# Kernel tuning notes

Measured on AMD Instinct MI355X. Metric: run time of the kernel, lower is better.

The kernel has to match this reference:

```python
import jax, jax.numpy as jnp
import numpy as np

N, E, DIN, HID, H, ED = 50000, 800000, 128, 64, 4, 5
Z_IDX = 3          # impedance column
PHYS_W = 1.0       # physics_weight
NEG_SLOPE = 0.2    # GATv2 leaky_relu slope


def gat_layer(x, src, dst, ea, Wl, bl, Wr, br, We, att, temp, bias, concat):
    """PhysicsGATv2Conv (add_self_loops=False, eval mode / no dropout)."""
    n = x.shape[0]
    Hh, C = att.shape
    xl = (x @ Wl + bl).reshape(n, Hh, C)   # lin_l -> source features
    xr = (x @ Wr + br).reshape(n, Hh, C)   # lin_r -> target features
    # physics-enhanced edge attr: overwrite last column with temp * w / |Z|
    z = jnp.clip(ea[:, Z_IDX], 1e-6, None)
    ea = ea.at[:, -1].set(temp * PHYS_W / z)
    e = (ea @ We).reshape(-1, Hh, C)       # lin_edge (no bias)
    m = jax.nn.leaky_relu(xl[src] + xr[dst] + e, NEG_SLOPE)  # [E,H,C]
    logit = jnp.einsum('ehc,hc->eh', m, att)                 # [E,H]
    # segment softmax over incoming edges of each target node
    lmax = jax.ops.segment_max(logit, dst, num_segments=n)
    w = jnp.exp(logit - lmax[dst])
    den = jax.ops.segment_sum(w, dst, num_segments=n)
    a = w / (den[dst] + 1e-16)
    out = jax.ops.segment_sum(xl[src] * a[:, :, None], dst, num_segments=n)
    out = out.reshape(n, Hh * C) if concat else out.mean(axis=1)
    return out + bias


def layer_norm(x, w, b):
    mu = x.mean(-1, keepdims=True)
    v = ((x - mu) ** 2).mean(-1, keepdims=True)
    return (x - mu) * jax.lax.rsqrt(v + 1e-5) * w + b


def setup_inputs() -> dict:
    key = jax.random.key(0)
    ks = iter(jax.random.split(key, 40))
    nk = lambda: next(ks)
    d = {}
    d['x'] = jax.random.normal(nk(), (N, DIN), jnp.float32)
    d['edge_index'] = jax.random.randint(nk(), (2, E), 0, N)
    d['edge_attr'] = jax.random.uniform(nk(), (E, ED), jnp.float32)
    hd = HID * H
    cfg = [(DIN, True), (hd, True), (hd, False)]
    for i, (din, concat) in enumerate(cfg):
        dout = hd if concat else HID
        d[f'Wl{i}'] = jax.random.normal(nk(), (din, hd), jnp.float32) / np.sqrt(din)
        d[f'bl{i}'] = 0.01 * jax.random.normal(nk(), (hd,), jnp.float32)
        d[f'Wr{i}'] = jax.random.normal(nk(), (din, hd), jnp.float32) / np.sqrt(din)
        d[f'br{i}'] = 0.01 * jax.random.normal(nk(), (hd,), jnp.float32)
        d[f'We{i}'] = jax.random.normal(nk(), (ED, hd), jnp.float32) / np.sqrt(ED)
        d[f'att{i}'] = jax.random.normal(nk(), (H, HID), jnp.float32) / np.sqrt(HID)
        d[f'temp{i}'] = jnp.float32(1.0)
        d[f'bias{i}'] = 0.01 * jax.random.normal(nk(), (dout,), jnp.float32)
        d[f'lnw{i}'] = jnp.ones((dout,), jnp.float32)
        d[f'lnb{i}'] = jnp.zeros((dout,), jnp.float32)
    d['pw0'] = jax.random.normal(nk(), (DIN, hd), jnp.float32) / np.sqrt(DIN)
    d['pb0'] = jnp.zeros((hd,), jnp.float32)
    d['pw2'] = jax.random.normal(nk(), (hd, HID), jnp.float32) / np.sqrt(hd)
    d['pb2'] = jnp.zeros((HID,), jnp.float32)
    return d


def reference(x, edge_index, edge_attr,
              Wl0, bl0, Wr0, br0, We0, att0, temp0, bias0, lnw0, lnb0,
              Wl1, bl1, Wr1, br1, We1, att1, temp1, bias1, lnw1, lnb1,
              Wl2, bl2, Wr2, br2, We2, att2, temp2, bias2, lnw2, lnb2,
              pw0, pb0, pw2, pb2):
    src, dst = edge_index[0], edge_index[1]
    # layer 0: 128 -> 256 (concat), residual projected
    h = gat_layer(x, src, dst, edge_attr, Wl0, bl0, Wr0, br0, We0, att0, temp0, bias0, True)
    h = layer_norm(h, lnw0, lnb0) + (x @ pw0 + pb0)
    h = jax.nn.elu(h)
    # layer 1: 256 -> 256 (concat), identity residual
    h1 = gat_layer(h, src, dst, edge_attr, Wl1, bl1, Wr1, br1, We1, att1, temp1, bias1, True)
    h = layer_norm(h1, lnw1, lnb1) + h
    h = jax.nn.elu(h)
    # layer 2: 256 -> 64 (head-mean), residual projected, no activation
    h2 = gat_layer(h, src, dst, edge_attr, Wl2, bl2, Wr2, br2, We2, att2, temp2, bias2, False)
    out = layer_norm(h2, lnw2, lnb2) + (h @ pw2 + pb2)
    return out
```

## Files before the change

kernel.cpp:

```cpp
#include <hip/hip_runtime.h>
#include <math.h>

#define NN 50000
#define EE 800000
#define NB 196

typedef _Float16 half8 __attribute__((ext_vector_type(8)));
typedef _Float16 hv4  __attribute__((ext_vector_type(4)));
typedef _Float16 hv2  __attribute__((ext_vector_type(2)));
typedef __fp16 fp16v2 __attribute__((ext_vector_type(2)));
typedef float floatx16 __attribute__((ext_vector_type(16)));
typedef float fv4 __attribute__((ext_vector_type(4)));

__device__ __forceinline__ float fexp2(float x) { return __builtin_amdgcn_exp2f(x); }

template<int CTRL>
__device__ __forceinline__ float dppadd(float x) {
    int t = __builtin_amdgcn_update_dpp(0, __float_as_int(x), CTRL, 0xf, 0xf, false);
    return x + __int_as_float(t);
}
__device__ __forceinline__ float red16(float x) {
    x = dppadd<0x121>(x);
    x = dppadd<0x122>(x);
    x = dppadd<0x124>(x);
    x = dppadd<0x128>(x);
    return x;
}

__device__ __forceinline__ unsigned int dup16(float x) {
    unsigned short b = __builtin_bit_cast(unsigned short, (_Float16)x);
    return (unsigned int)b * 0x10001u;
}
__device__ __forceinline__ unsigned int duph(float x) {
#if __has_builtin(__builtin_amdgcn_cvt_pkrtz)
    fp16v2 p = __builtin_amdgcn_cvt_pkrtz(x, x);
    return __builtin_bit_cast(unsigned int, p);
#else
    return dup16(x);
#endif
}
__device__ __forceinline__ hv4 b4(unsigned int u) {
    hv2 p = __builtin_bit_cast(hv2, u);
    return (hv4){p[0], p[1], p[0], p[1]};
}
__device__ __forceinline__ float dot4h(hv4 a, hv4 b, float c) {
    hv2 al = {a[0], a[1]}, ah = {a[2], a[3]};
    hv2 bl = {b[0], b[1]}, bh = {b[2], b[3]};
#if __has_builtin(__builtin_amdgcn_fdot2)
    return __builtin_amdgcn_fdot2(al, bl, __builtin_amdgcn_fdot2(ah, bh, c, false), false);
#else
    return c + (float)a[0]*(float)b[0] + (float)a[1]*(float)b[1]
             + (float)a[2]*(float)b[2] + (float)a[3]*(float)b[3];
#endif
}

__global__ __launch_bounds__(256) void swizzleA(
    const float* __restrict__ A, _Float16* __restrict__ Asw, int M, int K)
{
    int wave = threadIdx.x >> 6, lane = threadIdx.x & 63;
    int tile = blockIdx.x;
    int kc = blockIdx.y * 4 + wave;
    int KC = K >> 4;
    if (kc >= KC) return;
    int row = tile * 32 + (lane & 31);
    int k0 = kc * 16 + (lane >> 5) * 8;
    float4 v0 = make_float4(0.f, 0.f, 0.f, 0.f);
    float4 v1 = make_float4(0.f, 0.f, 0.f, 0.f);
    if (row < M) {
        const float* p = A + (size_t)row * K + k0;
        v0 = *(const float4*)p;
        v1 = *(const float4*)(p + 4);
    }
    half8 o;
    o[0] = (_Float16)v0.x; o[1] = (_Float16)v0.y;
    o[2] = (_Float16)v0.z; o[3] = (_Float16)v0.w;
    o[4] = (_Float16)v1.x; o[5] = (_Float16)v1.y;
    o[6] = (_Float16)v1.z; o[7] = (_Float16)v1.w;
    *(half8*)(Asw + (((size_t)tile * KC + kc) * 64 + lane) * 8) = o;
}

__global__ __launch_bounds__(256) void prep_weights(
    const float* __restrict__ s0, const float* __restrict__ s1,
    const float* __restrict__ s2, const float* __restrict__ s3,
    const float* __restrict__ s4, const float* __restrict__ s5,
    const float* __restrict__ s6, const float* __restrict__ s7,
    _Float16* __restrict__ catB0, _Float16* __restrict__ catB1,
    _Float16* __restrict__ catB2,
    const float* __restrict__ bl0, const float* __restrict__ br0,
    const float* __restrict__ pb0, const float* __restrict__ bl1,
    const float* __restrict__ br1, const float* __restrict__ bl2,
    const float* __restrict__ br2, const float* __restrict__ pb2,
    float* __restrict__ cb0, float* __restrict__ cb1, float* __restrict__ cb2,
    const float* __restrict__ We0a, const float* __restrict__ We1a,
    const float* __restrict__ We2a, const float* __restrict__ att0a,
    const float* __restrict__ att1a, const float* __restrict__ att2a,
    _Float16* __restrict__ Weh)
{
    int b = blockIdx.x;
    if (b == 192) {
        const float* Ws[3] = {We0a, We1a, We2a};
        const float* As[3] = {att0a, att1a, att2a};
        for (int t = threadIdx.x; t < 4608; t += 256) {
            int l = t / 1536, o = t - l * 1536;
            float v = (o < 1280) ? Ws[l][o] : As[l][o - 1280];
            Weh[t] = (_Float16)v;
        }
        return;
    }
    if (b >= 184) {
        int t = (b - 184) * 256 + threadIdx.x;
        if (t < 768) {
            cb0[t] = (t < 256) ? bl0[t] : (t < 512) ? br0[t - 256] : pb0[t - 512];
        } else if (t < 1280) {
            int u = t - 768;
            cb1[u] = (u < 256) ? bl1[u] : br1[u - 256];
        } else if (t < 1856) {
            int u = t - 1280;
            cb2[u] = (u < 256) ? bl2[u] : (u < 512) ? br2[u - 256] : pb2[u - 512];
        }
        return;
    }
    int wave = threadIdx.x >> 6, lane = threadIdx.x & 63;
    int pair = b * 4 + wave;
    const int cum[9] = {0, 64, 128, 192, 320, 448, 576, 704, 736};
    int job = 0;
    while (pair >= cum[job + 1]) ++job;
    const float* srcs[8] = {s0, s1, s2, s3, s4, s5, s6, s7};
    const int KCs[8] = {8, 8, 8, 16, 16, 16, 16, 16};
    const int NCs[8] = {256, 256, 256, 256, 256, 256, 256, 64};
    const int ntb[8] = {0, 8, 16, 0, 8, 0, 8, 16};
    _Float16* dsts[8] = {catB0, catB0, catB0, catB1, catB1, catB2, catB2, catB2};
    int p = pair - cum[job];
    int KC = KCs[job], NC = NCs[job];
    int nt = p / KC, kc = p - nt * KC;
    int n = (nt >> 1) * 64 + ((lane & 31) * 2) + (nt & 1);
    int k0 = kc * 16 + (lane >> 5) * 8;
    const float* B = srcs[job];
    half8 o;
#pragma unroll
    for (int jj = 0; jj < 8; ++jj)
        o[jj] = (_Float16)B[(size_t)(k0 + jj) * NC + n];
    int ntG = ntb[job] + nt;
    *(half8*)(dsts[job] + (((size_t)ntG * KC + kc) * 64 + lane) * 8) = o;
}

__global__ __launch_bounds__(256) void gemm_mfma(
    const _Float16* __restrict__ Asw, const _Float16* __restrict__ Bsw,
    const float* __restrict__ bias, _Float16* __restrict__ C,
    int M, int K, int NC)
{
    const int wave = threadIdx.x >> 6, lane = threadIdx.x & 63;
    const int KC = K >> 4;
    const int rt0 = blockIdx.x * 2;
    const int NG = NC >> 6;
    int g = blockIdx.y * 4 + wave;
    if (g >= NG) g = NG - 1;

    const half8* Ap0 = (const half8*)Asw + (size_t)rt0 * KC * 64 + lane;
    const half8* Ap1 = Ap0 + (size_t)KC * 64;
    const half8* Bp0 = (const half8*)Bsw + (size_t)(2 * g) * KC * 64 + lane;
    const half8* Bp1 = Bp0 + (size_t)KC * 64;

    floatx16 accE0 = {0.f}, accE1 = {0.f}, accO0 = {0.f}, accO1 = {0.f};

#pragma unroll 4
    for (int kc = 0; kc < KC; ++kc) {
        half8 a0 = Ap0[(size_t)kc * 64];
        half8 a1 = Ap1[(size_t)kc * 64];
        half8 b0 = Bp0[(size_t)kc * 64];
        half8 b1 = Bp1[(size_t)kc * 64];
        accE0 = __builtin_amdgcn_mfma_f32_32x32x16_f16(a0, b0, accE0, 0, 0, 0);
        accE1 = __builtin_amdgcn_mfma_f32_32x32x16_f16(a1, b0, accE1, 0, 0, 0);
        accO0 = __builtin_amdgcn_mfma_f32_32x32x16_f16(a0, b1, accO0, 0, 0, 0);
        accO1 = __builtin_amdgcn_mfma_f32_32x32x16_f16(a1, b1, accO1, 0, 0, 0);
    }

    const int nlane = lane & 31, hs = lane >> 5;
    int colb = g * 64 + nlane * 2;
    float be = bias[colb], bo = bias[colb + 1];
#pragma unroll
    for (int r = 0; r < 16; ++r) {
        int rowin = (r & 3) + 8 * (r >> 2) + 4 * hs;
        int row0 = rt0 * 32 + rowin;
        int row1 = row0 + 32;
        if (row0 < M) {
            hv2 pe;
            pe[0] = (_Float16)(accE0[r] + be);
            pe[1] = (_Float16)(accO0[r] + bo);
            *(hv2*)(C + (size_t)row0 * NC + colb) = pe;
        }
        if (row1 < M) {
            hv2 po;
            po[0] = (_Float16)(accE1[r] + be);
            po[1] = (_Float16)(accO1[r] + bo);
            *(hv2*)(C + (size_t)row1 * NC + colb) = po;
        }
    }
}

__global__ __launch_bounds__(256) void hist_kernel(const int* __restrict__ dst,
                                                   int* __restrict__ deg)
{
    int e = blockIdx.x * 256 + threadIdx.x;
    if (e < EE) atomicAdd(&deg[dst[e]], 1);
}

__global__ __launch_bounds__(256) void scan_local(const int* __restrict__ deg,
                                                  int* __restrict__ rowoff,
                                                  int* __restrict__ part)
{
    __shared__ int sd[256];
    int tid = threadIdx.x;
    int i = blockIdx.x * 256 + tid;
    int v = (i < NN) ? deg[i] : 0;
    sd[tid] = v;
    __syncthreads();
    for (int off = 1; off < 256; off <<= 1) {
        int t = (tid >= off) ? sd[tid - off] : 0;
        __syncthreads();
        sd[tid] += t;
        __syncthreads();
    }
    if (i < NN) rowoff[i] = sd[tid] - v;
    if (tid == 255) part[blockIdx.x] = sd[255];
}

__global__ __launch_bounds__(256) void scan_part(int* __restrict__ part,
                                                 int* __restrict__ rowoff)
{
    __shared__ int sd[256];
    int tid = threadIdx.x;
    int v = (tid < NB) ? part[tid] : 0;
    sd[tid] = v;
    __syncthreads();
    for (int off = 1; off < 256; off <<= 1) {
        int t = (tid >= off) ? sd[tid - off] : 0;
        __syncthreads();
        sd[tid] += t;
        __syncthreads();
    }
    if (tid < NB) part[tid] = sd[tid] - v;
    if (tid == 0) rowoff[NN] = EE;
}

__global__ __launch_bounds__(256) void scan_add(int* __restrict__ rowoff,
                                                const int* __restrict__ part,
                                                int* __restrict__ cursor)
{
    int i = blockIdx.x * 256 + threadIdx.x;
    if (i < NN) {
        rowoff[i] += part[blockIdx.x];
        cursor[i] = 0;
    }
}

__global__ __launch_bounds__(256) void scatter_kernel(
    const int* __restrict__ src, const int* __restrict__ dst,
    const float* __restrict__ ea, const int* __restrict__ rowoff,
    int* __restrict__ cursor, int2* __restrict__ sep,
    unsigned int* __restrict__ apk)
{
    int e = blockIdx.x * 256 + threadIdx.x;
    if (e < EE) {
        int d = dst[e];
        int pos = rowoff[d] + atomicAdd(&cursor[d], 1);
        const float* p = ea + (size_t)e * 5;
        int2 o2;
        o2.x = src[e];
        o2.y = __float_as_int(1.0f / fmaxf(p[3], 1e-6f));
        sep[pos] = o2;
        uint4 o;
        o.x = dup16(p[0]); o.y = dup16(p[1]);
        o.z = dup16(p[2]); o.w = dup16(p[3]);
        *(uint4*)(apk + (size_t)pos * 4) = o;
    }
}

__global__ __launch_bounds__(256) void build_qtab(
    const int2* __restrict__ sep,
    const float* __restrict__ tA, unsigned int* __restrict__ qA,
    const float* __restrict__ tB, unsigned int* __restrict__ qB)
{
    int e = blockIdx.x * 256 + threadIdx.x;
    if (e >= EE) return;
    float er = __int_as_float(sep[e].y);
    {
        float q = tA[0] * er;
        float qs = fminf(q, 64.f);
        float inv = (q > 64.f) ? 64.f * __builtin_amdgcn_rcpf(q) : 1.0f;
        float sl = fmaxf(q * 0.015625f, 1.f) * 1.44269504088896340736f;
        uint4 o;
        o.x = dup16(qs);
        o.y = dup16(inv);
        o.z = __builtin_bit_cast(unsigned int, sl);
        o.w = 0u;
        *(uint4*)(qA + (size_t)e * 4) = o;
    }
    if (qB) {
        float q = tB[0] * er;
        float qs = fminf(q, 64.f);
        float inv = (q > 64.f) ? 64.f * __builtin_amdgcn_rcpf(q) : 1.0f;
        float sl = fmaxf(q * 0.015625f, 1.f) * 1.44269504088896340736f;
        uint4 o;
        o.x = dup16(qs);
        o.y = dup16(inv);
        o.z = __builtin_bit_cast(unsigned int, sl);
        o.w = 0u;
        *(uint4*)(qB + (size_t)e * 4) = o;
    }
}

template<int MODE, int RSTRIDE>
__global__ __launch_bounds__(256) void fused_attn_ln(
    const int* __restrict__ rowoff, const int2* __restrict__ sep,
    const unsigned int* __restrict__ apk, const unsigned int* __restrict__ qtab,
    const _Float16* __restrict__ xlp, const _Float16* __restrict__ Wh,
    const float* __restrict__ bias, const float* __restrict__ lnw,
    const float* __restrict__ lnb,
    const _Float16* __restrict__ residH, _Float16* __restrict__ h16,
    float* __restrict__ outF, _Float16* __restrict__ aswOut)
{
    int v = __builtin_amdgcn_readfirstlane(blockIdx.x * 4 + (threadIdx.x >> 6));
    int lane = threadIdx.x & 63;
    if (v >= NN) return;
    int grp = lane >> 4;
    int sub = lane & 15;
    int j = grp * 64 + sub * 4;

    hv4 ww0h = *(const hv4*)(Wh + j);
    hv4 ww1h = *(const hv4*)(Wh + 256 + j);
    hv4 ww2h = *(const hv4*)(Wh + 512 + j);
    hv4 ww3h = *(const hv4*)(Wh + 768 + j);
    hv4 ww4h = *(const hv4*)(Wh + 1024 + j);
    hv4 atvh = *(const hv4*)(Wh + 1280 + j);
    hv4 xrvh = *(const hv4*)(xlp + (size_t)v * RSTRIDE + 256 + j);
    const _Float16 s02 = (_Float16)0.2f;
    const hv4 sl02 = {s02, s02, s02, s02};
    const float L2E = 1.44269504088896340736f;

    float mxd = -INFINITY, dend = 0.f;
    fv4 acc = {0.f, 0.f, 0.f, 0.f};

    int beg = __builtin_amdgcn_readfirstlane(rowoff[v]);
    int end = __builtin_amdgcn_readfirstlane(rowoff[v + 1]);
    int i = beg;
    for (; i + 4 <= end; i += 4) {
        int s[4]; uint4 ap[4], qt[4]; hv4 xh[4]; float l[4];
#pragma unroll
        for (int u = 0; u < 4; ++u) {
            int2 sv = sep[i + u];
            s[u] = __builtin_amdgcn_readfirstlane(sv.x);
            ap[u] = *(const uint4*)(apk + (size_t)(i + u) * 4);
            qt[u] = *(const uint4*)(qtab + (size_t)(i + u) * 4);
        }
#pragma unroll
        for (int u = 0; u < 4; ++u)
            xh[u] = *(const hv4*)(xlp + (size_t)s[u] * RSTRIDE + j);
#pragma unroll
        for (int u = 0; u < 4; ++u) {
            hv4 t = xh[u] + xrvh;
            t += b4(ap[u].x) * ww0h;
            t += b4(ap[u].y) * ww1h;
            t += b4(ap[u].z) * ww2h;
            t += b4(ap[u].w) * ww3h;
            hv4 m = b4(qt[u].x) * ww4h;
            m += b4(qt[u].y) * t;
            hv4 mn = m * sl02;
            m = __builtin_elementwise_max(m, mn);
            l[u] = dot4h(m, atvh, 0.f);
        }
#pragma unroll
        for (int u = 0; u < 4; ++u)
            l[u] = red16(l[u]) * __builtin_bit_cast(float, qt[u].z);
        float nm = fmaxf(fmaxf(l[0], l[1]), fmaxf(l[2], l[3]));
        nm = fmaxf(nm, mxd);
        float sc = fexp2(mxd - nm);
        float e0 = fexp2(l[0] - nm);
        float e1 = fexp2(l[1] - nm);
        float e2 = fexp2(l[2] - nm);
        float e3 = fexp2(l[3] - nm);
        mxd = nm;
        dend = dend * sc + ((e0 + e1) + (e2 + e3));
        hv4 X = xh[0] * b4(duph(e0));
        X += xh[1] * b4(duph(e1));
        X += xh[2] * b4(duph(e2));
        X += xh[3] * b4(duph(e3));
        fv4 Xf = __builtin_convertvector(X, fv4);
        acc = acc * sc + Xf;
    }
    for (; i < end; ++i) {
        int2 sv = sep[i];
        int s0 = __builtin_amdgcn_readfirstlane(sv.x);
        uint4 ap = *(const uint4*)(apk + (size_t)i * 4);
        uint4 qt = *(const uint4*)(qtab + (size_t)i * 4);
        hv4 xh = *(const hv4*)(xlp + (size_t)s0 * RSTRIDE + j);
        hv4 t = xh + xrvh;
        t += b4(ap.x) * ww0h;
        t += b4(ap.y) * ww1h;
        t += b4(ap.z) * ww2h;
        t += b4(ap.w) * ww3h;
        hv4 m = b4(qt.x) * ww4h;
        m += b4(qt.y) * t;
        hv4 mn = m * sl02;
        m = __builtin_elementwise_max(m, mn);
        float l0 = dot4h(m, atvh, 0.f);
        l0 = red16(l0) * __builtin_bit_cast(float, qt.z);
        float nm = fmaxf(mxd, l0);
        float sc = fexp2(mxd - nm);
        float e0 = fexp2(l0 - nm);
        mxd = nm;
        dend = dend * sc + e0;
        fv4 xf = __builtin_convertvector(xh, fv4);
        acc = acc * sc + xf * e0;
    }

    float inv = __builtin_amdgcn_rcpf(dend + 1e-16f);
    if (MODE <= 1) {
        fv4 bb = *(const fv4*)(bias + j);
        fv4 o = acc * inv + bb;
        float s  = (o[0] + o[1]) + (o[2] + o[3]);
        fv4 oq = o * o;
        float s2 = (oq[0] + oq[1]) + (oq[2] + oq[3]);
        s = red16(s);   s += __shfl_xor(s, 16, 64);  s += __shfl_xor(s, 32, 64);
        s2 = red16(s2); s2 += __shfl_xor(s2, 16, 64); s2 += __shfl_xor(s2, 32, 64);
        float mu = s * (1.f / 256.f);
        float var = s2 * (1.f / 256.f) - mu * mu;
        float rs = __builtin_amdgcn_rsqf(var + 1e-5f);
        fv4 lw = *(const fv4*)(lnw + j);
        fv4 lb = *(const fv4*)(lnb + j);
        fv4 rr;
        if (MODE == 0)
            rr = __builtin_convertvector(
                *(const hv4*)(residH + (size_t)v * RSTRIDE + j), fv4);
        else
            rr = __builtin_convertvector(
                *(const hv4*)(residH + (size_t)v * 256 + j), fv4);
        fv4 y = (o - mu) * rs * lw + lb + rr;
        y[0] = (y[0] > 0.f) ? y[0] : fexp2(y[0] * L2E) - 1.f;
        y[1] = (y[1] > 0.f) ? y[1] : fexp2(y[1] * L2E) - 1.f;
        y[2] = (y[2] > 0.f) ? y[2] : fexp2(y[2] * L2E) - 1.f;
        y[3] = (y[3] > 0.f) ? y[3] : fexp2(y[3] * L2E) - 1.f;
        hv4 yh = __builtin_convertvector(y, hv4);
        if (MODE == 0)
            *(hv4*)(h16 + (size_t)v * 256 + j) = yh;
        int kc = j >> 4, half = (j >> 3) & 1, off = j & 7;
        size_t idx = (((size_t)(v >> 5) * 16 + kc) * 64 + (v & 31) + 32 * half) * 8 + off;
        *(hv4*)(aswOut + idx) = yh;
    } else {
        fv4 r = acc * inv;
        r[0] += __shfl_xor(r[0], 16, 64); r[0] += __shfl_xor(r[0], 32, 64);
        r[1] += __shfl_xor(r[1], 16, 64); r[1] += __shfl_xor(r[1], 32, 64);
        r[2] += __shfl_xor(r[2], 16, 64); r[2] += __shfl_xor(r[2], 32, 64);
        r[3] += __shfl_xor(r[3], 16, 64); r[3] += __shfl_xor(r[3], 32, 64);
        fv4 bb = *(const fv4*)(bias + sub * 4);
        fv4 o = r * 0.25f + bb;
        float s  = (o[0] + o[1]) + (o[2] + o[3]);
        fv4 oq = o * o;
        float s2 = (oq[0] + oq[1]) + (oq[2] + oq[3]);
        s = red16(s);
        s2 = red16(s2);
        float mu = s * (1.f / 64.f);
        float var = s2 * (1.f / 64.f) - mu * mu;
        float rs = __builtin_amdgcn_rsqf(var + 1e-5f);
        fv4 lw = *(const fv4*)(lnw + sub * 4);
        fv4 lb = *(const fv4*)(lnb + sub * 4);
        fv4 rr = __builtin_convertvector(
            *(const hv4*)(residH + (size_t)v * RSTRIDE + sub * 4), fv4);
        fv4 y = (o - mu) * rs * lw + lb + rr;
        if (grp == 0)
            *(fv4*)(outF + (size_t)v * 64 + sub * 4) = y;
    }
}

extern "C" void kernel_launch(void* const* d_in, const int* in_sizes, int n_in,
                              void* d_out, int out_size, void* d_ws, size_t ws_size,
                              hipStream_t stream)
{
    const float* x    = (const float*)d_in[0];
    const int*   eidx = (const int*)d_in[1];
    const float* ea   = (const float*)d_in[2];
    const int* src = eidx;
    const int* dst = eidx + EE;

    const float *Wl[3], *bl[3], *Wr[3], *br[3], *We[3], *att[3], *temp[3],
                *bias[3], *lnw[3], *lnb[3];
    for (int i = 0; i < 3; ++i) {
        int b = 3 + i * 10;
        Wl[i]   = (const float*)d_in[b + 0];
        bl[i]   = (const float*)d_in[b + 1];
        Wr[i]   = (const float*)d_in[b + 2];
        br[i]   = (const float*)d_in[b + 3];
        We[i]   = (const float*)d_in[b + 4];
        att[i]  = (const float*)d_in[b + 5];
        temp[i] = (const float*)d_in[b + 6];
        bias[i] = (const float*)d_in[b + 7];
        lnw[i]  = (const float*)d_in[b + 8];
        lnb[i]  = (const float*)d_in[b + 9];
    }
    const float* pw0 = (const float*)d_in[33];
    const float* pb0 = (const float*)d_in[34];
    const float* pw2 = (const float*)d_in[35];
    const float* pb2 = (const float*)d_in[36];

    char* w = (char*)d_ws;
    _Float16* h16 = (_Float16*)w; w += (size_t)NN * 256 * 2;
    char*  gbase = w;         w += (size_t)NN * 256 * 4;
    _Float16* xlr = (_Float16*)w; w += (size_t)NN * 768 * 2;
    unsigned int* apk = (unsigned int*)w; w += (size_t)EE * 16;
    int2* sep    = (int2*)w;  w += (size_t)EE * 8;
    unsigned int* qtab1 = (unsigned int*)w; w += (size_t)EE * 16;
    int* rowoff  = (int*)w;   w += (size_t)(NN + 16) * 4;
    int* cursor  = (int*)w;   w += (size_t)NN * 4;
    int* part    = (int*)w;   w += 1024;
    w = (char*)(((uintptr_t)w + 255) & ~(uintptr_t)255);
    _Float16* catB0 = (_Float16*)w; w += 196608;
    _Float16* catB1 = (_Float16*)w; w += 262144;
    _Float16* catB2 = (_Float16*)w; w += 294912;
    float* cb0 = (float*)w; w += 768 * 4;
    float* cb1 = (float*)w; w += 512 * 4;
    float* cb2 = (float*)w; w += 576 * 4;
    _Float16* Weh = (_Float16*)w; w += 4608 * 2;
    _Float16* Asw = (_Float16*)gbase;
    unsigned int* qslot = (unsigned int*)(gbase + 26000000);

    dim3 blk(256);
    dim3 grid_e((EE + 255) / 256);
    dim3 grid_nw((NN + 3) / 4);
    dim3 grid_nb(NB);
    const int MT2 = 782;

    hipMemsetAsync(cursor, 0, (size_t)NN * 4, stream);
    hipLaunchKernelGGL(hist_kernel, grid_e, blk, 0, stream, dst, cursor);
    hipLaunchKernelGGL(scan_local, grid_nb, blk, 0, stream, cursor, rowoff, part);
    hipLaunchKernelGGL(scan_part, dim3(1), blk, 0, stream, part, rowoff);
    hipLaunchKernelGGL(scan_add, grid_nb, blk, 0, stream, rowoff, part, cursor);
    hipLaunchKernelGGL(scatter_kernel, grid_e, blk, 0, stream,
                       src, dst, ea, rowoff, cursor, sep, apk);

    hipLaunchKernelGGL(build_qtab, grid_e, blk, 0, stream,
                       sep, temp[0], qslot, temp[1], qtab1);

    hipLaunchKernelGGL(prep_weights, dim3(193), blk, 0, stream,
                       Wl[0], Wr[0], pw0, Wl[1], Wr[1], Wl[2], Wr[2], pw2,
                       catB0, catB1, catB2,
                       bl[0], br[0], pb0, bl[1], br[1], bl[2], br[2], pb2,
                       cb0, cb1, cb2,
                       We[0], We[1], We[2], att[0], att[1], att[2], Weh);

    swizzleA<<<dim3(1564, 2), blk, 0, stream>>>(x, Asw, NN, 128);
    gemm_mfma<<<dim3(MT2, 3), blk, 0, stream>>>(
        Asw, catB0, cb0, xlr, NN, 128, 768);
    fused_attn_ln<0, 768><<<grid_nw, blk, 0, stream>>>(
        rowoff, sep, apk, qslot, xlr, Weh,
        bias[0], lnw[0], lnb[0], xlr + 512, h16, nullptr, Asw);

    hipLaunchKernelGGL(build_qtab, grid_e, blk, 0, stream,
                       sep, temp[2], qslot, nullptr, nullptr);

    gemm_mfma<<<dim3(MT2, 2), blk, 0, stream>>>(
        Asw, catB1, cb1, xlr, NN, 256, 512);
    fused_attn_ln<1, 512><<<grid_nw, blk, 0, stream>>>(
        rowoff, sep, apk, qtab1, xlr, Weh + 1536,
        bias[1], lnw[1], lnb[1], h16, nullptr, nullptr, Asw);

    gemm_mfma<<<dim3(MT2, 3), blk, 0, stream>>>(
        Asw, catB2, cb2, xlr, NN, 256, 576);
    fused_attn_ln<2, 576><<<grid_nw, blk, 0, stream>>>(
        rowoff, sep, apk, qslot, xlr, Weh + 3072,
        bias[2], lnw[2], lnb[2], xlr + 512, nullptr, (float*)d_out, nullptr);
}
```

Baseline: 615.6 us.

## Process nodes in descending-degree order and fold qtab build into scatter

Adds a degree histogram, a scan and an ordering kernel that lists node ids sorted by in-degree, largest first. The fused attention kernels now look up their node through this order, so high-degree nodes start first and tail imbalance across waves shrinks. Separately, the first two layers' q-tables are now written inside the scatter kernel, removing one edge-sized pass that reread sep. The cost is two extra small kernels, an extra indirection per wave, and output rows that are no longer written in order, which loses some locality.

Measured after the change: 915.7 us. 1.49x slower.

```diff
diff --git a/kernel.cpp b/kernel.cpp
--- a/kernel.cpp
+++ b/kernel.cpp
@@ -52,6 +52,19 @@
     return c + (float)a[0]*(float)b[0] + (float)a[1]*(float)b[1]
              + (float)a[2]*(float)b[2] + (float)a[3]*(float)b[3];
 #endif
+}
+
+__device__ __forceinline__ uint4 qrec(float tt, float er) {
+    float q = tt * er;
+    float qs = fminf(q, 64.f);
+    float inv = (q > 64.f) ? 64.f * __builtin_amdgcn_rcpf(q) : 1.0f;
+    float sl = fmaxf(q * 0.015625f, 1.f) * 1.44269504088896340736f;
+    uint4 o;
+    o.x = dup16(qs);
+    o.y = dup16(inv);
+    o.z = __builtin_bit_cast(unsigned int, sl);
+    o.w = 0u;
+    return o;
 }
 
 __global__ __launch_bounds__(256) void swizzleA(
@@ -199,8 +212,10 @@
 }
 
 __global__ __launch_bounds__(256) void hist_kernel(const int* __restrict__ dst,
-                                                   int* __restrict__ deg)
-{
+                                                   int* __restrict__ deg,
+                                                   int* __restrict__ dbin)
+{
+    if (blockIdx.x == 0) dbin[threadIdx.x] = dbin[256 + threadIdx.x] = 0;
     int e = blockIdx.x * 256 + threadIdx.x;
     if (e < EE) atomicAdd(&deg[dst[e]], 1);
 }
@@ -245,12 +260,46 @@
 
 __global__ __launch_bounds__(256) void scan_add(int* __restrict__ rowoff,
                                                 const int* __restrict__ part,
-                                                int* __restrict__ cursor)
+                                                int* __restrict__ cursor,
+                                                int* __restrict__ dbin)
 {
     int i = blockIdx.x * 256 + threadIdx.x;
     if (i < NN) {
         rowoff[i] += part[blockIdx.x];
+        int d = cursor[i];
         cursor[i] = 0;
+        atomicAdd(&dbin[d < 255 ? d : 255], 1);
+    }
+}
+
+__global__ __launch_bounds__(256) void dscan(const int* __restrict__ dbin,
+                                             int* __restrict__ dboff)
+{
+    __shared__ int sd[256];
+    int tid = threadIdx.x;
+    sd[tid] = dbin[255 - tid];
+    __syncthreads();
+    for (int off = 1; off < 256; off <<= 1) {
+        int t = (tid >= off) ? sd[tid - off] : 0;
+        __syncthreads();
+        sd[tid] += t;
+        __syncthreads();
+    }
+    if (tid < 255) dboff[254 - tid] = sd[tid];
+    else dboff[255] = 0;
+}
+
+__global__ __launch_bounds__(256) void dorder(const int* __restrict__ rowoff,
+                                              const int* __restrict__ dboff,
+                                              int* __restrict__ dcur,
+                                              int* __restrict__ order)
+{
+    int i = blockIdx.x * 256 + threadIdx.x;
+    if (i < NN) {
+        int d = rowoff[i + 1] - rowoff[i];
+        if (d > 255) d = 255;
+        int pos = dboff[d] + atomicAdd(&dcur[d], 1);
+        order[pos] = i;
     }
 }
 
@@ -258,60 +307,42 @@
     const int* __restrict__ src, const int* __restrict__ dst,
     const float* __restrict__ ea, const int* __restrict__ rowoff,
     int* __restrict__ cursor, int2* __restrict__ sep,
-    unsigned int* __restrict__ apk)
+    unsigned int* __restrict__ apk,
+    const float* __restrict__ t0, unsigned int* __restrict__ q0,
+    const float* __restrict__ t1, unsigned int* __restrict__ q1)
 {
     int e = blockIdx.x * 256 + threadIdx.x;
     if (e < EE) {
         int d = dst[e];
         int pos = rowoff[d] + atomicAdd(&cursor[d], 1);
         const float* p = ea + (size_t)e * 5;
+        float er = 1.0f / fmaxf(p[3], 1e-6f);
         int2 o2;
         o2.x = src[e];
-        o2.y = __float_as_int(1.0f / fmaxf(p[3], 1e-6f));
+        o2.y = __float_as_int(er);
         sep[pos] = o2;
         uint4 o;
         o.x = dup16(p[0]); o.y = dup16(p[1]);
         o.z = dup16(p[2]); o.w = dup16(p[3]);
         *(uint4*)(apk + (size_t)pos * 4) = o;
+        *(uint4*)(q0 + (size_t)pos * 4) = qrec(t0[0], er);
+        *(uint4*)(q1 + (size_t)pos * 4) = qrec(t1[0], er);
     }
 }
 
 __global__ __launch_bounds__(256) void build_qtab(
     const int2* __restrict__ sep,
-    const float* __restrict__ tA, unsigned int* __restrict__ qA,
-    const float* __restrict__ tB, unsigned int* __restrict__ qB)
+    const float* __restrict__ tA, unsigned int* __restrict__ qA)
 {
     int e = blockIdx.x * 256 + threadIdx.x;
     if (e >= EE) return;
     float er = __int_as_float(sep[e].y);
-    {
-        float q = tA[0] * er;
-        float qs = fminf(q, 64.f);
-        float inv = (q > 64.f) ? 64.f * __builtin_amdgcn_rcpf(q) : 1.0f;
-        float sl = fmaxf(q * 0.015625f, 1.f) * 1.44269504088896340736f;
-        uint4 o;
-        o.x = dup16(qs);
-        o.y = dup16(inv);
-        o.z = __builtin_bit_cast(unsigned int, sl);
-        o.w = 0u;
-        *(uint4*)(qA + (size_t)e * 4) = o;
-    }
-    if (qB) {
-        float q = tB[0] * er;
-        float qs = fminf(q, 64.f);
-        float inv = (q > 64.f) ? 64.f * __builtin_amdgcn_rcpf(q) : 1.0f;
-        float sl = fmaxf(q * 0.015625f, 1.f) * 1.44269504088896340736f;
-        uint4 o;
-        o.x = dup16(qs);
-        o.y = dup16(inv);
-        o.z = __builtin_bit_cast(unsigned int, sl);
-        o.w = 0u;
-        *(uint4*)(qB + (size_t)e * 4) = o;
-    }
+    *(uint4*)(qA + (size_t)e * 4) = qrec(tA[0], er);
 }
 
 template<int MODE, int RSTRIDE>
 __global__ __launch_bounds__(256) void fused_attn_ln(
+    const int* __restrict__ order,
     const int* __restrict__ rowoff, const int2* __restrict__ sep,
     const unsigned int* __restrict__ apk, const unsigned int* __restrict__ qtab,
     const _Float16* __restrict__ xlp, const _Float16* __restrict__ Wh,
@@ -320,7 +351,8 @@
     const _Float16* __restrict__ residH, _Float16* __restrict__ h16,
     float* __restrict__ outF, _Float16* __restrict__ aswOut)
 {
-    int v = __builtin_amdgcn_readfirstlane(blockIdx.x * 4 + (threadIdx.x >> 6));
+    int slot = blockIdx.x * 4 + (threadIdx.x >> 6);
+    int v = __builtin_amdgcn_readfirstlane(order[slot]);
     int lane = threadIdx.x & 63;
     if (v >= NN) return;
     int grp = lane >> 4;
@@ -512,6 +544,9 @@
     int* rowoff  = (int*)w;   w += (size_t)(NN + 16) * 4;
     int* cursor  = (int*)w;   w += (size_t)NN * 4;
     int* part    = (int*)w;   w += 1024;
+    int* order   = (int*)w;   w += (size_t)NN * 4;
+    int* dbin    = (int*)w;   w += 512 * 4;
+    int* dboff   = (int*)w;   w += 256 * 4;
     w = (char*)(((uintptr_t)w + 255) & ~(uintptr_t)255);
     _Float16* catB0 = (_Float16*)w; w += 196608;
     _Float16* catB1 = (_Float16*)w; w += 262144;
@@ -530,15 +565,16 @@
     const int MT2 = 782;
 
     hipMemsetAsync(cursor, 0, (size_t)NN * 4, stream);
-    hipLaunchKernelGGL(hist_kernel, grid_e, blk, 0, stream, dst, cursor);
+    hipLaunchKernelGGL(hist_kernel, grid_e, blk, 0, stream, dst, cursor, dbin);
     hipLaunchKernelGGL(scan_local, grid_nb, blk, 0, stream, cursor, rowoff, part);
     hipLaunchKernelGGL(scan_part, dim3(1), blk, 0, stream, part, rowoff);
-    hipLaunchKernelGGL(scan_add, grid_nb, blk, 0, stream, rowoff, part, cursor);
+    hipLaunchKernelGGL(scan_add, grid_nb, blk, 0, stream, rowoff, part, cursor, dbin);
+    hipLaunchKernelGGL(dscan, dim3(1), blk, 0, stream, dbin, dboff);
     hipLaunchKernelGGL(scatter_kernel, grid_e, blk, 0, stream,
-                       src, dst, ea, rowoff, cursor, sep, apk);
-
-    hipLaunchKernelGGL(build_qtab, grid_e, blk, 0, stream,
-                       sep, temp[0], qslot, temp[1], qtab1);
+                       src, dst, ea, rowoff, cursor, sep, apk,
+                       temp[0], qslot, temp[1], qtab1);
+    hipLaunchKernelGGL(dorder, grid_nb, blk, 0, stream,
+                       rowoff, dboff, dbin + 256, order);
 
     hipLaunchKernelGGL(prep_weights, dim3(193), blk, 0, stream,
                        Wl[0], Wr[0], pw0, Wl[1], Wr[1], Wl[2], Wr[2], pw2,
@@ -551,21 +587,21 @@
     gemm_mfma<<<dim3(MT2, 3), blk, 0, stream>>>(
         Asw, catB0, cb0, xlr, NN, 128, 768);
     fused_attn_ln<0, 768><<<grid_nw, blk, 0, stream>>>(
-        rowoff, sep, apk, qslot, xlr, Weh,
+        order, rowoff, sep, apk, qslot, xlr, Weh,
         bias[0], lnw[0], lnb[0], xlr + 512, h16, nullptr, Asw);
 
     hipLaunchKernelGGL(build_qtab, grid_e, blk, 0, stream,
-                       sep, temp[2], qslot, nullptr, nullptr);
+                       sep, temp[2], qslot);
 
     gemm_mfma<<<dim3(MT2, 2), blk, 0, stream>>>(
         Asw, catB1, cb1, xlr, NN, 256, 512);
     fused_attn_ln<1, 512><<<grid_nw, blk, 0, stream>>>(
-        rowoff, sep, apk, qtab1, xlr, Weh + 1536,
+        order, rowoff, sep, apk, qtab1, xlr, Weh + 1536,
         bias[1], lnw[1], lnb[1], h16, nullptr, nullptr, Asw);
 
     gemm_mfma<<<dim3(MT2, 3), blk, 0, stream>>>(
         Asw, catB2, cb2, xlr, NN, 256, 576);
     fused_attn_ln<2, 576><<<grid_nw, blk, 0, stream>>>(
-        rowoff, sep, apk, qslot, xlr, Weh + 3072,
+        order, rowoff, sep, apk, qslot, xlr, Weh + 3072,
         bias[2], lnw[2], lnb[2], xlr + 512, nullptr, (float*)d_out, nullptr);
 }
```
